# Kernel optimization log

Hardware: AMD Instinct MI355X
Metric: run time of the kernel (lower is better)

## Reference

```python
import jax, jax.numpy as jnp
import numpy as np

N_HEAD = 8


def setup_inputs() -> dict:
    key = jax.random.key(0)
    k1, k2, k3 = jax.random.split(key, 3)
    B, D, L = 4, 1024, 2048  # channels-first: (batch, feature, seq)
    q = jax.random.normal(k1, (B, D, L), dtype=jnp.float32)
    k = jax.random.normal(k2, (B, D, L), dtype=jnp.float32)
    v = jax.random.normal(k3, (B, D, L), dtype=jnp.float32)
    gamma = jnp.ones((), dtype=jnp.float32)  # nn.Parameter scalar, init 1.0
    return {"q": q, "k": k, "v": v, "gamma": gamma}


def reference(q, k, v, gamma):
    # q, k, v: (B, D, L) channels-first. Head split on feature dim (-2).
    B, Dq, Lq = q.shape
    Dv, Lk = v.shape[-2], v.shape[-1]
    h = N_HEAD
    dq = Dq // h  # per-head query/key dim
    dv = Dv // h  # per-head value dim
    qh = q.reshape(B, h, dq, Lq)
    kh = k.reshape(B, h, dq, Lk)
    vh = v.reshape(B, h, dv, Lk)
    # scale = sqrt(q.size(-2)) AFTER head split, i.e. sqrt(d_head)
    scale = 1.0 / jnp.sqrt(jnp.asarray(dq, dtype=q.dtype))
    # qk: (B, h, Lq, Lk)
    qk = jnp.einsum('bhdq,bhdl->bhql', qh, kh) * scale
    sm = jax.nn.softmax(qk, axis=-1)
    # torch: (sm.unsqueeze(-3) * v.unsqueeze(-2)).sum(-1) == contraction over Lk
    ret = jnp.einsum('bhql,bhdl->bhdq', sm, vh)  # (B, h, dv, Lq)
    ret = ret.reshape(B, Dv, Lq)  # torch: ret.view(-1, v_shape[-2], q_shape[-1])
    return gamma * ret
```

## Files before the change

### kernel.cpp

```cpp
#include <hip/hip_runtime.h>

#define SEQ 2048
#define DHEAD 128
#define BK 32
#define NBH 32

typedef __attribute__((ext_vector_type(8))) short bf16x8;
typedef __attribute__((ext_vector_type(4))) short bf16x4;
typedef __attribute__((ext_vector_type(16))) float f32x16;
typedef __attribute__((ext_vector_type(4))) unsigned int u32x4;

__device__ __forceinline__ unsigned short f2bf(float f) {
    unsigned u = __builtin_bit_cast(unsigned, f);
    u += 0x7fffu + ((u >> 16) & 1u);
    return (unsigned short)(u >> 16);
}

__device__ __forceinline__ void gload16(const unsigned short* g, unsigned short* l) {
    __builtin_amdgcn_global_load_lds((const __attribute__((address_space(1))) void*)g,
                                     (__attribute__((address_space(3))) void*)l, 16, 0, 0);
}

__global__ __launch_bounds__(256)
void cvt_kernel(const float* __restrict__ kin, const float* __restrict__ vin,
                unsigned short* __restrict__ kout, unsigned short* __restrict__ vout) {
    const int tid = threadIdx.x;
    if (blockIdx.x < 1024) {
        __shared__ unsigned short tileT[DHEAD][66];
        const int bh = blockIdx.x & 31;
        const int l0 = (blockIdx.x >> 5) * 64;
        const float* ip = kin + (size_t)bh * DHEAD * SEQ;
        unsigned short* opx = kout + ((size_t)bh * SEQ + l0) * DHEAD;
        const int l4 = (tid & 15) * 4;
        const int dq = tid >> 4;
        for (int pass = 0; pass < 8; ++pass) {
            int d = pass * 16 + dq;
            float4 f = *(const float4*)&ip[(size_t)d * SEQ + l0 + l4];
            unsigned lo = (unsigned)f2bf(f.x) | ((unsigned)f2bf(f.y) << 16);
            unsigned hi = (unsigned)f2bf(f.z) | ((unsigned)f2bf(f.w) << 16);
            *(unsigned*)&tileT[d][l4]     = lo;
            *(unsigned*)&tileT[d][l4 + 2] = hi;
        }
        __syncthreads();
        const int lw = tid >> 2;
        const int cw = tid & 3;
        const int ksw = (lw & 7) ^ (((lw >> 3) & 3) << 1);
        for (int j = 0; j < 4; ++j) {
            int pc = j * 4 + cw;
            int lc = pc ^ ksw;
            unsigned short tmp[8];
            for (int k2 = 0; k2 < 8; ++k2) tmp[k2] = tileT[lc * 8 + k2][lw];
            *(bf16x8*)&opx[(size_t)lw * DHEAD + pc * 8] = *(bf16x8*)tmp;
        }
    } else {
        size_t f = ((size_t)(blockIdx.x - 1024) * 256 + tid) * 8;
        int bh  = (int)(f >> 18);
        int rem = (int)(f & 262143);
        int kt  = rem >> 12;
        int r2  = rem & 4095;
        int dv  = r2 >> 5;
        int e0  = r2 & 31;
        const float* src = vin + ((size_t)bh * DHEAD + dv) * SEQ + kt * BK + e0;
        float4 a = *(const float4*)src;
        float4 b = *(const float4*)(src + 4);
        unsigned short p0[4] = {f2bf(a.x), f2bf(a.y), f2bf(a.z), f2bf(a.w)};
        unsigned short p1[4] = {f2bf(b.x), f2bf(b.y), f2bf(b.z), f2bf(b.w)};
        const int aa = e0 >> 4;
        const int bb = (e0 >> 3) & 1;
        const int w  = ((dv >> 1) & 3) ^ ((dv >> 3) & 3);
        size_t rowb = ((size_t)bh * (SEQ / BK) + kt) * (DHEAD * BK) + (size_t)dv * BK;
        *(bf16x4*)&vout[rowb + (size_t)(((2 * aa) ^ w) * 8 + 4 * bb)]     = *(bf16x4*)p0;
        *(bf16x4*)&vout[rowb + (size_t)(((2 * aa + 1) ^ w) * 8 + 4 * bb)] = *(bf16x4*)p1;
    }
}

__global__ __launch_bounds__(128, 1)
void attn_main(const float* __restrict__ q,
               const unsigned short* __restrict__ kTg,
               const unsigned short* __restrict__ vW,
               const float* __restrict__ gamma,
               float* __restrict__ out) {
    __shared__ __attribute__((aligned(16))) unsigned short kS[2][BK * DHEAD];
    __shared__ __attribute__((aligned(16))) unsigned short vS[2][DHEAD * BK];

    const int tid  = threadIdx.x;
    const int wv   = tid >> 6;
    const int lane = tid & 63;
    const int c5   = lane & 31;
    const int hi   = lane >> 5;

    const int bh  = blockIdx.x & 31;
    const int qlb = blockIdx.x >> 5;
    const size_t base = (size_t)bh * SEQ * DHEAD;

    const float* qp = q + base;
    const unsigned short* kb = kTg + base;
    const unsigned short* vb = vW + base;
    float* op = out + base;

    const int ql0 = qlb * 128 + wv * 64;
    const float SCL = 0.08838834764831845f * 1.44269504088896340f;

#pragma unroll
    for (int i = 0; i < 4; ++i) {
        gload16(kb + (size_t)(tid + i * 128) * 8, &kS[0][(tid + i * 128) * 8]);
        gload16(vb + (size_t)(tid + i * 128) * 8, &vS[0][(tid + i * 128) * 8]);
    }

    bf16x8 qf0[8], qf1[8];
#pragma unroll
    for (int s = 0; s < 8; ++s) {
        bf16x8 t0, t1;
#pragma unroll
        for (int j = 0; j < 8; ++j) {
            const size_t drow = (size_t)(s * 16 + hi * 8 + j) * SEQ;
            t0[j] = (short)f2bf(qp[drow + ql0 + c5] * SCL);
            t1[j] = (short)f2bf(qp[drow + ql0 + 32 + c5] * SCL);
        }
        qf0[s] = t0;
        qf1[s] = t1;
    }

    f32x16 acc0[4], acc1[4];
#pragma unroll
    for (int t = 0; t < 4; ++t)
#pragma unroll
        for (int i = 0; i < 16; ++i) { acc0[t][i] = 0.f; acc1[t][i] = 0.f; }
    float lp0 = 0.f, lp1 = 0.f;

    const int ksw = (c5 & 7) ^ (((c5 >> 3) & 3) << 1);
    const int vsw = ((c5 >> 1) & 3) ^ ((c5 >> 3) & 3);

    for (int kt = 0; kt < SEQ / BK; ++kt) {
        const int cur = kt & 1;
        __syncthreads();

        if (kt + 1 < SEQ / BK) {
            const unsigned short* kg = kb + (size_t)(kt + 1) * (BK * DHEAD);
            const unsigned short* vg = vb + (size_t)(kt + 1) * (DHEAD * BK);
#pragma unroll
            for (int i = 0; i < 4; ++i) {
                gload16(kg + (size_t)(tid + i * 128) * 8, &kS[cur ^ 1][(tid + i * 128) * 8]);
                gload16(vg + (size_t)(tid + i * 128) * 8, &vS[cur ^ 1][(tid + i * 128) * 8]);
            }
        }

        f32x16 sT0, sT1;
#pragma unroll
        for (int i = 0; i < 16; ++i) { sT0[i] = 0.f; sT1[i] = 0.f; }
#pragma unroll
        for (int s = 0; s < 8; ++s) {
            bf16x8 kf = *(const bf16x8*)&kS[cur][c5 * DHEAD + (((2 * s + hi) ^ ksw) * 8)];
            sT0 = __builtin_amdgcn_mfma_f32_32x32x16_bf16(kf, qf0[s], sT0, 0, 0, 0);
            sT1 = __builtin_amdgcn_mfma_f32_32x32x16_bf16(kf, qf1[s], sT1, 0, 0, 0);
        }

        unsigned pw0[8], pw1[8];
#pragma unroll
        for (int i = 0; i < 8; ++i) {
            float a0 = exp2f(sT0[2 * i]);
            float b0 = exp2f(sT0[2 * i + 1]);
            float a1 = exp2f(sT1[2 * i]);
            float b1 = exp2f(sT1[2 * i + 1]);
            lp0 += a0 + b0;
            lp1 += a1 + b1;
            unsigned r0, r1;
            asm("v_cvt_pk_bf16_f32 %0, %1, %2" : "=v"(r0) : "v"(a0), "v"(b0));
            asm("v_cvt_pk_bf16_f32 %0, %1, %2" : "=v"(r1) : "v"(a1), "v"(b1));
            pw0[i] = r0;
            pw1[i] = r1;
        }
        bf16x8 p0a = __builtin_bit_cast(bf16x8, (u32x4){pw0[0], pw0[1], pw0[2], pw0[3]});
        bf16x8 p0b = __builtin_bit_cast(bf16x8, (u32x4){pw0[4], pw0[5], pw0[6], pw0[7]});
        bf16x8 p1a = __builtin_bit_cast(bf16x8, (u32x4){pw1[0], pw1[1], pw1[2], pw1[3]});
        bf16x8 p1b = __builtin_bit_cast(bf16x8, (u32x4){pw1[4], pw1[5], pw1[6], pw1[7]});

#pragma unroll
        for (int t = 0; t < 4; ++t) {
            bf16x8 va = *(const bf16x8*)&vS[cur][(32 * t + c5) * BK + (((0 + hi) ^ vsw) * 8)];
            bf16x8 vb8 = *(const bf16x8*)&vS[cur][(32 * t + c5) * BK + (((2 + hi) ^ vsw) * 8)];
            acc0[t] = __builtin_amdgcn_mfma_f32_32x32x16_bf16(va,  p0a, acc0[t], 0, 0, 0);
            acc0[t] = __builtin_amdgcn_mfma_f32_32x32x16_bf16(vb8, p0b, acc0[t], 0, 0, 0);
            acc1[t] = __builtin_amdgcn_mfma_f32_32x32x16_bf16(va,  p1a, acc1[t], 0, 0, 0);
            acc1[t] = __builtin_amdgcn_mfma_f32_32x32x16_bf16(vb8, p1b, acc1[t], 0, 0, 0);
        }
    }

    const float gm = gamma[0];
    {
        const float L0 = lp0 + __shfl_xor(lp0, 32);
        const float sc0 = gm / L0;
        const int ql = ql0 + c5;
#pragma unroll
        for (int t = 0; t < 4; ++t)
#pragma unroll
            for (int r = 0; r < 16; ++r) {
                int dvr = 32 * t + (r & 3) + 8 * (r >> 2) + 4 * hi;
                op[(size_t)dvr * SEQ + ql] = acc0[t][r] * sc0;
            }
    }
    {
        const float L1 = lp1 + __shfl_xor(lp1, 32);
        const float sc1 = gm / L1;
        const int ql = ql0 + 32 + c5;
#pragma unroll
        for (int t = 0; t < 4; ++t)
#pragma unroll
            for (int r = 0; r < 16; ++r) {
                int dvr = 32 * t + (r & 3) + 8 * (r >> 2) + 4 * hi;
                op[(size_t)dvr * SEQ + ql] = acc1[t][r] * sc1;
            }
    }
}

extern "C" void kernel_launch(void* const* d_in, const int* in_sizes, int n_in,
                              void* d_out, int out_size, void* d_ws, size_t ws_size,
                              hipStream_t stream) {
    (void)in_sizes; (void)n_in; (void)out_size; (void)ws_size;
    const float* q = (const float*)d_in[0];
    const float* k = (const float*)d_in[1];
    const float* v = (const float*)d_in[2];
    const float* g = (const float*)d_in[3];
    float* out = (float*)d_out;

    const size_t PER_T = (size_t)NBH * SEQ * DHEAD;
    unsigned short* kws = (unsigned short*)d_ws;
    unsigned short* vws = kws + PER_T;

    cvt_kernel<<<dim3(1024 + 4096), dim3(256), 0, stream>>>(k, v, kws, vws);
    attn_main<<<dim3(512), dim3(128), 0, stream>>>(q, kws, vws, g, out);
}
```

Baseline: 254.6 us.

## Split key sequence across two wave pairs per block and merge partial results

Doubles the block to 256 threads. Two halves of the block each process half of the key/value sequence with their own double-buffered LDS tiles. The partial row sums and output accumulators are then reduced through shared memory before the store. This puts more waves on each CU, since only 512 blocks exist, to hide latency, at the cost of an extra LDS reduction and more shared memory. It also swaps exp2f for the raw v_exp_f32 instruction, adds s_setprio around the MFMA sections, and precomputes the LDS offsets.

```diff
diff --git a/kernel.cpp b/kernel.cpp
--- a/kernel.cpp
+++ b/kernel.cpp
@@ -4,6 +4,7 @@
 #define DHEAD 128
 #define BK 32
 #define NBH 32
+#define NTH 32
 
 typedef __attribute__((ext_vector_type(8))) short bf16x8;
 typedef __attribute__((ext_vector_type(4))) short bf16x4;
@@ -14,6 +15,12 @@
     unsigned u = __builtin_bit_cast(unsigned, f);
     u += 0x7fffu + ((u >> 16) & 1u);
     return (unsigned short)(u >> 16);
+}
+
+__device__ __forceinline__ float fexp2(float x) {
+    float r;
+    asm("v_exp_f32 %0, %1" : "=v"(r) : "v"(x));
+    return r;
 }
 
 __device__ __forceinline__ void gload16(const unsigned short* g, unsigned short* l) {
@@ -74,20 +81,23 @@
     }
 }
 
-__global__ __launch_bounds__(128, 1)
+__global__ __launch_bounds__(256, 2)
 void attn_main(const float* __restrict__ q,
                const unsigned short* __restrict__ kTg,
                const unsigned short* __restrict__ vW,
                const float* __restrict__ gamma,
                float* __restrict__ out) {
-    __shared__ __attribute__((aligned(16))) unsigned short kS[2][BK * DHEAD];
-    __shared__ __attribute__((aligned(16))) unsigned short vS[2][DHEAD * BK];
+    __shared__ __attribute__((aligned(16))) unsigned short smem[32768];
 
     const int tid  = threadIdx.x;
     const int wv   = tid >> 6;
     const int lane = tid & 63;
     const int c5   = lane & 31;
     const int hi   = lane >> 5;
+    const int qw   = wv & 1;
+    const int sh   = wv >> 1;
+    const int th   = tid >> 7;
+    const int t7   = tid & 127;
 
     const int bh  = blockIdx.x & 31;
     const int qlb = blockIdx.x >> 5;
@@ -98,13 +108,19 @@
     const unsigned short* vb = vW + base;
     float* op = out + base;
 
-    const int ql0 = qlb * 128 + wv * 64;
+    const int ql0 = qlb * 128 + qw * 64;
     const float SCL = 0.08838834764831845f * 1.44269504088896340f;
 
-#pragma unroll
-    for (int i = 0; i < 4; ++i) {
-        gload16(kb + (size_t)(tid + i * 128) * 8, &kS[0][(tid + i * 128) * 8]);
-        gload16(vb + (size_t)(tid + i * 128) * 8, &vS[0][(tid + i * 128) * 8]);
+    const unsigned short* kb_h = kb + (size_t)(th * NTH) * (BK * DHEAD);
+    const unsigned short* vb_h = vb + (size_t)(th * NTH) * (DHEAD * BK);
+
+#define KBUF(h, b) (&smem[((h) * 2 + (b)) * 8192])
+#define VBUF(h, b) (&smem[((h) * 2 + (b)) * 8192 + 4096])
+
+#pragma unroll
+    for (int j = 0; j < 4; ++j) {
+        gload16(kb_h + (size_t)(t7 + j * 128) * 8, KBUF(th, 0) + (t7 + j * 128) * 8);
+        gload16(vb_h + (size_t)(t7 + j * 128) * 8, VBUF(th, 0) + (t7 + j * 128) * 8);
     }
 
     bf16x8 qf0[8], qf1[8];
@@ -130,87 +146,146 @@
 
     const int ksw = (c5 & 7) ^ (((c5 >> 3) & 3) << 1);
     const int vsw = ((c5 >> 1) & 3) ^ ((c5 >> 3) & 3);
-
-    for (int kt = 0; kt < SEQ / BK; ++kt) {
-        const int cur = kt & 1;
+    int koff[8], voffa[4], voffb[4];
+#pragma unroll
+    for (int s = 0; s < 8; ++s) koff[s] = c5 * DHEAD + (((2 * s + hi) ^ ksw) * 8);
+#pragma unroll
+    for (int t = 0; t < 4; ++t) {
+        voffa[t] = (32 * t + c5) * BK + (((0 + hi) ^ vsw) * 8);
+        voffb[t] = (32 * t + c5) * BK + (((2 + hi) ^ vsw) * 8);
+    }
+
+    auto body = [&](int i, int cur) {
         __syncthreads();
 
-        if (kt + 1 < SEQ / BK) {
-            const unsigned short* kg = kb + (size_t)(kt + 1) * (BK * DHEAD);
-            const unsigned short* vg = vb + (size_t)(kt + 1) * (DHEAD * BK);
-#pragma unroll
-            for (int i = 0; i < 4; ++i) {
-                gload16(kg + (size_t)(tid + i * 128) * 8, &kS[cur ^ 1][(tid + i * 128) * 8]);
-                gload16(vg + (size_t)(tid + i * 128) * 8, &vS[cur ^ 1][(tid + i * 128) * 8]);
+        if (i + 1 < NTH) {
+            const unsigned short* kg = kb_h + (size_t)(i + 1) * (BK * DHEAD);
+            const unsigned short* vg = vb_h + (size_t)(i + 1) * (DHEAD * BK);
+            unsigned short* kd = KBUF(th, cur ^ 1);
+            unsigned short* vd = VBUF(th, cur ^ 1);
+#pragma unroll
+            for (int j = 0; j < 4; ++j) {
+                gload16(kg + (size_t)(t7 + j * 128) * 8, kd + (t7 + j * 128) * 8);
+                gload16(vg + (size_t)(t7 + j * 128) * 8, vd + (t7 + j * 128) * 8);
             }
         }
 
+        const unsigned short* kT = KBUF(sh, cur);
+        const unsigned short* vT = VBUF(sh, cur);
+
         f32x16 sT0, sT1;
 #pragma unroll
-        for (int i = 0; i < 16; ++i) { sT0[i] = 0.f; sT1[i] = 0.f; }
+        for (int ii = 0; ii < 16; ++ii) { sT0[ii] = 0.f; sT1[ii] = 0.f; }
+        __builtin_amdgcn_s_setprio(1);
 #pragma unroll
         for (int s = 0; s < 8; ++s) {
-            bf16x8 kf = *(const bf16x8*)&kS[cur][c5 * DHEAD + (((2 * s + hi) ^ ksw) * 8)];
+            bf16x8 kf = *(const bf16x8*)&kT[koff[s]];
             sT0 = __builtin_amdgcn_mfma_f32_32x32x16_bf16(kf, qf0[s], sT0, 0, 0, 0);
             sT1 = __builtin_amdgcn_mfma_f32_32x32x16_bf16(kf, qf1[s], sT1, 0, 0, 0);
         }
+        __builtin_amdgcn_s_setprio(0);
 
         unsigned pw0[8], pw1[8];
 #pragma unroll
-        for (int i = 0; i < 8; ++i) {
-            float a0 = exp2f(sT0[2 * i]);
-            float b0 = exp2f(sT0[2 * i + 1]);
-            float a1 = exp2f(sT1[2 * i]);
-            float b1 = exp2f(sT1[2 * i + 1]);
+        for (int ii = 0; ii < 8; ++ii) {
+            float a0 = fexp2(sT0[2 * ii]);
+            float b0 = fexp2(sT0[2 * ii + 1]);
+            float a1 = fexp2(sT1[2 * ii]);
+            float b1 = fexp2(sT1[2 * ii + 1]);
             lp0 += a0 + b0;
             lp1 += a1 + b1;
             unsigned r0, r1;
             asm("v_cvt_pk_bf16_f32 %0, %1, %2" : "=v"(r0) : "v"(a0), "v"(b0));
             asm("v_cvt_pk_bf16_f32 %0, %1, %2" : "=v"(r1) : "v"(a1), "v"(b1));
-            pw0[i] = r0;
-            pw1[i] = r1;
+            pw0[ii] = r0;
+            pw1[ii] = r1;
         }
         bf16x8 p0a = __builtin_bit_cast(bf16x8, (u32x4){pw0[0], pw0[1], pw0[2], pw0[3]});
         bf16x8 p0b = __builtin_bit_cast(bf16x8, (u32x4){pw0[4], pw0[5], pw0[6], pw0[7]});
         bf16x8 p1a = __builtin_bit_cast(bf16x8, (u32x4){pw1[0], pw1[1], pw1[2], pw1[3]});
         bf16x8 p1b = __builtin_bit_cast(bf16x8, (u32x4){pw1[4], pw1[5], pw1[6], pw1[7]});
 
+        __builtin_amdgcn_s_setprio(1);
 #pragma unroll
         for (int t = 0; t < 4; ++t) {
-            bf16x8 va = *(const bf16x8*)&vS[cur][(32 * t + c5) * BK + (((0 + hi) ^ vsw) * 8)];
-            bf16x8 vb8 = *(const bf16x8*)&vS[cur][(32 * t + c5) * BK + (((2 + hi) ^ vsw) * 8)];
+            bf16x8 va  = *(const bf16x8*)&vT[voffa[t]];
+            bf16x8 vb8 = *(const bf16x8*)&vT[voffb[t]];
             acc0[t] = __builtin_amdgcn_mfma_f32_32x32x16_bf16(va,  p0a, acc0[t], 0, 0, 0);
             acc0[t] = __builtin_amdgcn_mfma_f32_32x32x16_bf16(vb8, p0b, acc0[t], 0, 0, 0);
             acc1[t] = __builtin_amdgcn_mfma_f32_32x32x16_bf16(va,  p1a, acc1[t], 0, 0, 0);
             acc1[t] = __builtin_amdgcn_mfma_f32_32x32x16_bf16(vb8, p1b, acc1[t], 0, 0, 0);
         }
-    }
-
+        __builtin_amdgcn_s_setprio(0);
+    };
+
+    for (int it = 0; it < NTH; it += 2) {
+        body(it, 0);
+        body(it + 1, 1);
+    }
+
+    float* lbuf = (float*)smem;
+    lbuf[(wv * 2 + 0) * 64 + lane] = lp0;
+    lbuf[(wv * 2 + 1) * 64 + lane] = lp1;
+    __syncthreads();
+    const int pw = wv ^ 2;
+    lp0 += lbuf[(pw * 2 + 0) * 64 + lane];
+    lp1 += lbuf[(pw * 2 + 1) * 64 + lane];
+    const float Lt0 = lp0 + __shfl_xor(lp0, 32);
+    const float Lt1 = lp1 + __shfl_xor(lp1, 32);
     const float gm = gamma[0];
-    {
-        const float L0 = lp0 + __shfl_xor(lp0, 32);
-        const float sc0 = gm / L0;
-        const int ql = ql0 + c5;
-#pragma unroll
-        for (int t = 0; t < 4; ++t)
-#pragma unroll
-            for (int r = 0; r < 16; ++r) {
-                int dvr = 32 * t + (r & 3) + 8 * (r >> 2) + 4 * hi;
-                op[(size_t)dvr * SEQ + ql] = acc0[t][r] * sc0;
-            }
-    }
-    {
-        const float L1 = lp1 + __shfl_xor(lp1, 32);
-        const float sc1 = gm / L1;
-        const int ql = ql0 + 32 + c5;
-#pragma unroll
-        for (int t = 0; t < 4; ++t)
-#pragma unroll
-            for (int r = 0; r < 16; ++r) {
-                int dvr = 32 * t + (r & 3) + 8 * (r >> 2) + 4 * hi;
-                op[(size_t)dvr * SEQ + ql] = acc1[t][r] * sc1;
-            }
-    }
+    const float sc0 = gm / Lt0;
+    const float sc1 = gm / Lt1;
+    __syncthreads();
+
+    float* abuf = (float*)smem;
+    if (sh == 0) {
+#pragma unroll
+        for (int r = 0; r < 16; ++r) {
+            abuf[(((wv * 2 + 0) * 2 + 0) * 16 + r) * 64 + lane] = acc0[2][r];
+            abuf[(((wv * 2 + 0) * 2 + 1) * 16 + r) * 64 + lane] = acc0[3][r];
+            abuf[(((wv * 2 + 1) * 2 + 0) * 16 + r) * 64 + lane] = acc1[2][r];
+            abuf[(((wv * 2 + 1) * 2 + 1) * 16 + r) * 64 + lane] = acc1[3][r];
+        }
+    } else {
+#pragma unroll
+        for (int r = 0; r < 16; ++r) {
+            abuf[(((wv * 2 + 0) * 2 + 0) * 16 + r) * 64 + lane] = acc0[0][r];
+            abuf[(((wv * 2 + 0) * 2 + 1) * 16 + r) * 64 + lane] = acc0[1][r];
+            abuf[(((wv * 2 + 1) * 2 + 0) * 16 + r) * 64 + lane] = acc1[0][r];
+            abuf[(((wv * 2 + 1) * 2 + 1) * 16 + r) * 64 + lane] = acc1[1][r];
+        }
+    }
+    __syncthreads();
+
+    if (sh == 0) {
+#pragma unroll
+        for (int r = 0; r < 16; ++r) {
+            float v00 = acc0[0][r] + abuf[(((pw * 2 + 0) * 2 + 0) * 16 + r) * 64 + lane];
+            float v01 = acc0[1][r] + abuf[(((pw * 2 + 0) * 2 + 1) * 16 + r) * 64 + lane];
+            float v10 = acc1[0][r] + abuf[(((pw * 2 + 1) * 2 + 0) * 16 + r) * 64 + lane];
+            float v11 = acc1[1][r] + abuf[(((pw * 2 + 1) * 2 + 1) * 16 + r) * 64 + lane];
+            int dvr = (r & 3) + 8 * (r >> 2) + 4 * hi;
+            op[(size_t)(dvr)      * SEQ + ql0 +      c5] = v00 * sc0;
+            op[(size_t)(32 + dvr) * SEQ + ql0 +      c5] = v01 * sc0;
+            op[(size_t)(dvr)      * SEQ + ql0 + 32 + c5] = v10 * sc1;
+            op[(size_t)(32 + dvr) * SEQ + ql0 + 32 + c5] = v11 * sc1;
+        }
+    } else {
+#pragma unroll
+        for (int r = 0; r < 16; ++r) {
+            float v00 = acc0[2][r] + abuf[(((pw * 2 + 0) * 2 + 0) * 16 + r) * 64 + lane];
+            float v01 = acc0[3][r] + abuf[(((pw * 2 + 0) * 2 + 1) * 16 + r) * 64 + lane];
+            float v10 = acc1[2][r] + abuf[(((pw * 2 + 1) * 2 + 0) * 16 + r) * 64 + lane];
+            float v11 = acc1[3][r] + abuf[(((pw * 2 + 1) * 2 + 1) * 16 + r) * 64 + lane];
+            int dvr = (r & 3) + 8 * (r >> 2) + 4 * hi;
+            op[(size_t)(64 + dvr) * SEQ + ql0 +      c5] = v00 * sc0;
+            op[(size_t)(96 + dvr) * SEQ + ql0 +      c5] = v01 * sc0;
+            op[(size_t)(64 + dvr) * SEQ + ql0 + 32 + c5] = v10 * sc1;
+            op[(size_t)(96 + dvr) * SEQ + ql0 + 32 + c5] = v11 * sc1;
+        }
+    }
+#undef KBUF
+#undef VBUF
 }
 
 extern "C" void kernel_launch(void* const* d_in, const int* in_sizes, int n_in,
@@ -228,5 +303,5 @@
     unsigned short* vws = kws + PER_T;
 
     cvt_kernel<<<dim3(1024 + 4096), dim3(256), 0, stream>>>(k, v, kws, vws);
-    attn_main<<<dim3(512), dim3(128), 0, stream>>>(q, kws, vws, g, out);
-}
+    attn_main<<<dim3(512), dim3(256), 0, stream>>>(q, kws, vws, g, out);
+}
```

Result: faster. 237.3 us (-6.8%).

## Prelayout K/V in MFMA fragment order and load directly from global, split D across waves

Applied to the files above, without the earlier changes.

The convert kernel now writes K and V in exact per-lane MFMA fragment order, so the attention kernel loads fragments straight from global memory into registers. This removes the LDS double buffer and its per-tile barriers. The block grows to 4 waves, with each pair of waves splitting the value dimension, which raises occupancy but makes every wave recompute QK^T and the softmax. It also adds s_setprio around the MFMA sections and replaces exp2f with a raw v_exp_f32 instruction.

```diff
diff --git a/kernel.cpp b/kernel.cpp
--- a/kernel.cpp
+++ b/kernel.cpp
@@ -16,9 +16,10 @@
     return (unsigned short)(u >> 16);
 }
 
-__device__ __forceinline__ void gload16(const unsigned short* g, unsigned short* l) {
-    __builtin_amdgcn_global_load_lds((const __attribute__((address_space(1))) void*)g,
-                                     (__attribute__((address_space(3))) void*)l, 16, 0, 0);
+__device__ __forceinline__ float fexp2(float x) {
+    float r;
+    asm("v_exp_f32 %0, %1" : "=v"(r) : "v"(x));
+    return r;
 }
 
 __global__ __launch_bounds__(256)
@@ -30,7 +31,6 @@
         const int bh = blockIdx.x & 31;
         const int l0 = (blockIdx.x >> 5) * 64;
         const float* ip = kin + (size_t)bh * DHEAD * SEQ;
-        unsigned short* opx = kout + ((size_t)bh * SEQ + l0) * DHEAD;
         const int l4 = (tid & 15) * 4;
         const int dq = tid >> 4;
         for (int pass = 0; pass < 8; ++pass) {
@@ -42,15 +42,18 @@
             *(unsigned*)&tileT[d][l4 + 2] = hi;
         }
         __syncthreads();
-        const int lw = tid >> 2;
-        const int cw = tid & 3;
-        const int ksw = (lw & 7) ^ (((lw >> 3) & 3) << 1);
-        for (int j = 0; j < 4; ++j) {
-            int pc = j * 4 + cw;
-            int lc = pc ^ ksw;
+        for (int m = 0; m < 4; ++m) {
+            int chunk = m * 256 + tid;
+            int c5  = chunk & 31;
+            int hi  = (chunk >> 5) & 1;
+            int s   = (chunk >> 6) & 7;
+            int ktl = chunk >> 9;
             unsigned short tmp[8];
-            for (int k2 = 0; k2 < 8; ++k2) tmp[k2] = tileT[lc * 8 + k2][lw];
-            *(bf16x8*)&opx[(size_t)lw * DHEAD + pc * 8] = *(bf16x8*)tmp;
+#pragma unroll
+            for (int j = 0; j < 8; ++j) tmp[j] = tileT[s * 16 + hi * 8 + j][ktl * 32 + c5];
+            size_t gkt = (size_t)(l0 >> 5) + ktl;
+            size_t off = ((size_t)bh * 64 + gkt) * 4096 + (size_t)(((s * 2 + hi) * 32 + c5) * 8);
+            *(bf16x8*)&kout[off] = *(bf16x8*)tmp;
         }
     } else {
         size_t f = ((size_t)(blockIdx.x - 1024) * 256 + tid) * 8;
@@ -67,45 +70,41 @@
         unsigned short p1[4] = {f2bf(b.x), f2bf(b.y), f2bf(b.z), f2bf(b.w)};
         const int aa = e0 >> 4;
         const int bb = (e0 >> 3) & 1;
-        const int w  = ((dv >> 1) & 3) ^ ((dv >> 3) & 3);
-        size_t rowb = ((size_t)bh * (SEQ / BK) + kt) * (DHEAD * BK) + (size_t)dv * BK;
-        *(bf16x4*)&vout[rowb + (size_t)(((2 * aa) ^ w) * 8 + 4 * bb)]     = *(bf16x4*)p0;
-        *(bf16x4*)&vout[rowb + (size_t)(((2 * aa + 1) ^ w) * 8 + 4 * bb)] = *(bf16x4*)p1;
+        const int u  = dv >> 5;
+        const int cv = dv & 31;
+        size_t tb = ((size_t)bh * 64 + kt) * 4096;
+        size_t o0 = tb + (size_t)((((u * 2 + aa) * 2 + 0) * 32 + cv) * 8 + 4 * bb);
+        size_t o1 = tb + (size_t)((((u * 2 + aa) * 2 + 1) * 32 + cv) * 8 + 4 * bb);
+        *(bf16x4*)&vout[o0] = *(bf16x4*)p0;
+        *(bf16x4*)&vout[o1] = *(bf16x4*)p1;
     }
 }
 
-__global__ __launch_bounds__(128, 1)
+__global__ __launch_bounds__(256, 2)
 void attn_main(const float* __restrict__ q,
-               const unsigned short* __restrict__ kTg,
-               const unsigned short* __restrict__ vW,
+               const unsigned short* __restrict__ kF,
+               const unsigned short* __restrict__ vF,
                const float* __restrict__ gamma,
                float* __restrict__ out) {
-    __shared__ __attribute__((aligned(16))) unsigned short kS[2][BK * DHEAD];
-    __shared__ __attribute__((aligned(16))) unsigned short vS[2][DHEAD * BK];
-
     const int tid  = threadIdx.x;
     const int wv   = tid >> 6;
     const int lane = tid & 63;
     const int c5   = lane & 31;
     const int hi   = lane >> 5;
+    const int qh   = wv & 1;
+    const int dh   = wv >> 1;
 
     const int bh  = blockIdx.x & 31;
     const int qlb = blockIdx.x >> 5;
     const size_t base = (size_t)bh * SEQ * DHEAD;
 
     const float* qp = q + base;
-    const unsigned short* kb = kTg + base;
-    const unsigned short* vb = vW + base;
+    const unsigned short* kb = kF + base;
+    const unsigned short* vb = vF + base;
     float* op = out + base;
 
-    const int ql0 = qlb * 128 + wv * 64;
+    const int ql0 = qlb * 128 + qh * 64;
     const float SCL = 0.08838834764831845f * 1.44269504088896340f;
-
-#pragma unroll
-    for (int i = 0; i < 4; ++i) {
-        gload16(kb + (size_t)(tid + i * 128) * 8, &kS[0][(tid + i * 128) * 8]);
-        gload16(vb + (size_t)(tid + i * 128) * 8, &vS[0][(tid + i * 128) * 8]);
-    }
 
     bf16x8 qf0[8], qf1[8];
 #pragma unroll
@@ -121,96 +120,86 @@
         qf1[s] = t1;
     }
 
-    f32x16 acc0[4], acc1[4];
-#pragma unroll
-    for (int t = 0; t < 4; ++t)
+    f32x16 acc0[2], acc1[2];
+#pragma unroll
+    for (int t = 0; t < 2; ++t)
 #pragma unroll
         for (int i = 0; i < 16; ++i) { acc0[t][i] = 0.f; acc1[t][i] = 0.f; }
     float lp0 = 0.f, lp1 = 0.f;
 
-    const int ksw = (c5 & 7) ^ (((c5 >> 3) & 3) << 1);
-    const int vsw = ((c5 >> 1) & 3) ^ ((c5 >> 3) & 3);
+    const int ko = lane * 8;
+    int voff[4];
+#pragma unroll
+    for (int t2 = 0; t2 < 2; ++t2)
+#pragma unroll
+        for (int a = 0; a < 2; ++a)
+            voff[t2 * 2 + a] = (((dh * 2 + t2) * 2 + a) * 2 + hi) * 256 + c5 * 8;
 
     for (int kt = 0; kt < SEQ / BK; ++kt) {
-        const int cur = kt & 1;
-        __syncthreads();
-
-        if (kt + 1 < SEQ / BK) {
-            const unsigned short* kg = kb + (size_t)(kt + 1) * (BK * DHEAD);
-            const unsigned short* vg = vb + (size_t)(kt + 1) * (DHEAD * BK);
-#pragma unroll
-            for (int i = 0; i < 4; ++i) {
-                gload16(kg + (size_t)(tid + i * 128) * 8, &kS[cur ^ 1][(tid + i * 128) * 8]);
-                gload16(vg + (size_t)(tid + i * 128) * 8, &vS[cur ^ 1][(tid + i * 128) * 8]);
-            }
-        }
+        const unsigned short* kT = kb + (size_t)kt * 4096;
+        const unsigned short* vT = vb + (size_t)kt * 4096;
+
+        bf16x8 kf[8], vf[4];
+#pragma unroll
+        for (int s = 0; s < 8; ++s) kf[s] = *(const bf16x8*)&kT[s * 512 + ko];
+#pragma unroll
+        for (int t = 0; t < 4; ++t) vf[t] = *(const bf16x8*)&vT[voff[t]];
 
         f32x16 sT0, sT1;
 #pragma unroll
-        for (int i = 0; i < 16; ++i) { sT0[i] = 0.f; sT1[i] = 0.f; }
+        for (int ii = 0; ii < 16; ++ii) { sT0[ii] = 0.f; sT1[ii] = 0.f; }
+        __builtin_amdgcn_s_setprio(1);
 #pragma unroll
         for (int s = 0; s < 8; ++s) {
-            bf16x8 kf = *(const bf16x8*)&kS[cur][c5 * DHEAD + (((2 * s + hi) ^ ksw) * 8)];
-            sT0 = __builtin_amdgcn_mfma_f32_32x32x16_bf16(kf, qf0[s], sT0, 0, 0, 0);
-            sT1 = __builtin_amdgcn_mfma_f32_32x32x16_bf16(kf, qf1[s], sT1, 0, 0, 0);
-        }
+            sT0 = __builtin_amdgcn_mfma_f32_32x32x16_bf16(kf[s], qf0[s], sT0, 0, 0, 0);
+            sT1 = __builtin_amdgcn_mfma_f32_32x32x16_bf16(kf[s], qf1[s], sT1, 0, 0, 0);
+        }
+        __builtin_amdgcn_s_setprio(0);
 
         unsigned pw0[8], pw1[8];
 #pragma unroll
-        for (int i = 0; i < 8; ++i) {
-            float a0 = exp2f(sT0[2 * i]);
-            float b0 = exp2f(sT0[2 * i + 1]);
-            float a1 = exp2f(sT1[2 * i]);
-            float b1 = exp2f(sT1[2 * i + 1]);
+        for (int ii = 0; ii < 8; ++ii) {
+            float a0 = fexp2(sT0[2 * ii]);
+            float b0 = fexp2(sT0[2 * ii + 1]);
+            float a1 = fexp2(sT1[2 * ii]);
+            float b1 = fexp2(sT1[2 * ii + 1]);
             lp0 += a0 + b0;
             lp1 += a1 + b1;
             unsigned r0, r1;
             asm("v_cvt_pk_bf16_f32 %0, %1, %2" : "=v"(r0) : "v"(a0), "v"(b0));
             asm("v_cvt_pk_bf16_f32 %0, %1, %2" : "=v"(r1) : "v"(a1), "v"(b1));
-            pw0[i] = r0;
-            pw1[i] = r1;
+            pw0[ii] = r0;
+            pw1[ii] = r1;
         }
         bf16x8 p0a = __builtin_bit_cast(bf16x8, (u32x4){pw0[0], pw0[1], pw0[2], pw0[3]});
         bf16x8 p0b = __builtin_bit_cast(bf16x8, (u32x4){pw0[4], pw0[5], pw0[6], pw0[7]});
         bf16x8 p1a = __builtin_bit_cast(bf16x8, (u32x4){pw1[0], pw1[1], pw1[2], pw1[3]});
         bf16x8 p1b = __builtin_bit_cast(bf16x8, (u32x4){pw1[4], pw1[5], pw1[6], pw1[7]});
 
-#pragma unroll
-        for (int t = 0; t < 4; ++t) {
-            bf16x8 va = *(const bf16x8*)&vS[cur][(32 * t + c5) * BK + (((0 + hi) ^ vsw) * 8)];
-            bf16x8 vb8 = *(const bf16x8*)&vS[cur][(32 * t + c5) * BK + (((2 + hi) ^ vsw) * 8)];
-            acc0[t] = __builtin_amdgcn_mfma_f32_32x32x16_bf16(va,  p0a, acc0[t], 0, 0, 0);
-            acc0[t] = __builtin_amdgcn_mfma_f32_32x32x16_bf16(vb8, p0b, acc0[t], 0, 0, 0);
-            acc1[t] = __builtin_amdgcn_mfma_f32_32x32x16_bf16(va,  p1a, acc1[t], 0, 0, 0);
-            acc1[t] = __builtin_amdgcn_mfma_f32_32x32x16_bf16(vb8, p1b, acc1[t], 0, 0, 0);
-        }
+        __builtin_amdgcn_s_setprio(1);
+#pragma unroll
+        for (int t2 = 0; t2 < 2; ++t2) {
+            acc0[t2] = __builtin_amdgcn_mfma_f32_32x32x16_bf16(vf[t2 * 2],     p0a, acc0[t2], 0, 0, 0);
+            acc0[t2] = __builtin_amdgcn_mfma_f32_32x32x16_bf16(vf[t2 * 2 + 1], p0b, acc0[t2], 0, 0, 0);
+            acc1[t2] = __builtin_amdgcn_mfma_f32_32x32x16_bf16(vf[t2 * 2],     p1a, acc1[t2], 0, 0, 0);
+            acc1[t2] = __builtin_amdgcn_mfma_f32_32x32x16_bf16(vf[t2 * 2 + 1], p1b, acc1[t2], 0, 0, 0);
+        }
+        __builtin_amdgcn_s_setprio(0);
     }
 
     const float gm = gamma[0];
-    {
-        const float L0 = lp0 + __shfl_xor(lp0, 32);
-        const float sc0 = gm / L0;
-        const int ql = ql0 + c5;
-#pragma unroll
-        for (int t = 0; t < 4; ++t)
-#pragma unroll
-            for (int r = 0; r < 16; ++r) {
-                int dvr = 32 * t + (r & 3) + 8 * (r >> 2) + 4 * hi;
-                op[(size_t)dvr * SEQ + ql] = acc0[t][r] * sc0;
-            }
-    }
-    {
-        const float L1 = lp1 + __shfl_xor(lp1, 32);
-        const float sc1 = gm / L1;
-        const int ql = ql0 + 32 + c5;
-#pragma unroll
-        for (int t = 0; t < 4; ++t)
-#pragma unroll
-            for (int r = 0; r < 16; ++r) {
-                int dvr = 32 * t + (r & 3) + 8 * (r >> 2) + 4 * hi;
-                op[(size_t)dvr * SEQ + ql] = acc1[t][r] * sc1;
-            }
-    }
+    const float L0 = lp0 + __shfl_xor(lp0, 32);
+    const float L1 = lp1 + __shfl_xor(lp1, 32);
+    const float sc0 = gm / L0;
+    const float sc1 = gm / L1;
+#pragma unroll
+    for (int t2 = 0; t2 < 2; ++t2)
+#pragma unroll
+        for (int r = 0; r < 16; ++r) {
+            int dvr = 32 * (dh * 2 + t2) + (r & 3) + 8 * (r >> 2) + 4 * hi;
+            op[(size_t)dvr * SEQ + ql0 + c5]      = acc0[t2][r] * sc0;
+            op[(size_t)dvr * SEQ + ql0 + 32 + c5] = acc1[t2][r] * sc1;
+        }
 }
 
 extern "C" void kernel_launch(void* const* d_in, const int* in_sizes, int n_in,
@@ -228,5 +217,5 @@
     unsigned short* vws = kws + PER_T;
 
     cvt_kernel<<<dim3(1024 + 4096), dim3(256), 0, stream>>>(k, v, kws, vws);
-    attn_main<<<dim3(512), dim3(128), 0, stream>>>(q, kws, vws, g, out);
-}
+    attn_main<<<dim3(512), dim3(256), 0, stream>>>(q, kws, vws, g, out);
+}
```

New measurement: 223.8 us. 1.14x faster.
